# Kernel tuning notes

Hardware: AMD Instinct MI355X
Metric: run time of the kernel (lower is better)

The kernel has to match this reference:

```python
import jax, jax.numpy as jnp
import numpy as np

B, S, D = 4, 16, 512          # batch, seq, attention_dim
V, T = 32000, 18              # vocab_size, tree_depth
INNER = V - 1                 # internal nodes of Huffman tree


def setup_inputs() -> dict:
    key = jax.random.key(0)
    k_att, k_w, k_idx, k_bit = jax.random.split(key, 4)
    att = jax.random.normal(k_att, (B, S, D), dtype=jnp.float32)
    weight = jax.random.normal(k_w, (INNER, D), dtype=jnp.float32) * 0.02
    path_index = jax.random.randint(k_idx, (V * T,), 0, INNER, dtype=jnp.int64)
    # left/right branch bits: sign=+1,bias=0 -> p ; sign=-1,bias=1 -> 1-p
    bits = jax.random.randint(k_bit, (V * T,), 0, 2).astype(jnp.float32)
    path_sign = 1.0 - 2.0 * bits
    path_bias = bits
    return {
        "att": att,
        "weight": weight,
        "path_index": path_index,
        "path_sign": path_sign,
        "path_bias": path_bias,
        "vocab_size": V,
        "tree_depth": T,
    }


def reference(att, weight, path_index, path_sign, path_bias, vocab_size, tree_depth):
    # h: sigmoid of linear projection onto internal-node vectors  [B,S,INNER]
    h = jax.nn.sigmoid(jnp.einsum("bsd,nd->bsn", att, weight))
    # gather per-(token,depth) internal-node probs, flip via sign/bias
    g = jnp.take(h, path_index, axis=-1) * path_sign + path_bias  # [B,S,V*T]
    Hm = g.reshape(att.shape[0], -1, vocab_size, tree_depth)      # [B,S,V,T]
    return jnp.sum(jnp.log(Hm), axis=-1)                          # [B,S,V]
```

## Files before the change

kernel.cpp:

```cpp
#include <hip/hip_runtime.h>
#include <hip/hip_bf16.h>

#define BS    64
#define DDIM  512
#define NV    32000
#define TD    18
#define INNER 31999
#define NPAD  32000

typedef __attribute__((ext_vector_type(8))) short short8;
typedef __attribute__((ext_vector_type(4))) float floatx4;

__device__ __forceinline__ float bf16_to_f32(unsigned short u) {
    union { unsigned int i; float f; } v; v.i = ((unsigned int)u) << 16; return v.f;
}
__device__ __forceinline__ unsigned short f32_to_bf16(float f) {
    union { float f; unsigned int i; } v; v.f = f;
    unsigned int r = v.i + 0x7FFFu + ((v.i >> 16) & 1u);
    return (unsigned short)(r >> 16);
}

__global__ __launch_bounds__(256) void cvt_att(
    const float4* __restrict__ att, ushort4* __restrict__ attb)
{
    int i = blockIdx.x * 256 + threadIdx.x;
    float4 a = att[i];
    ushort4 r;
    r.x = f32_to_bf16(a.x); r.y = f32_to_bf16(a.y);
    r.z = f32_to_bf16(a.z); r.w = f32_to_bf16(a.w);
    attb[i] = r;
}

__global__ __launch_bounds__(512, 4) void gemm_logsig(
    const unsigned short* __restrict__ attb,
    const float* __restrict__ weight,
    unsigned int* __restrict__ pairsT)
{
    __shared__ floatx4 cmb[4][64][4];
    const int tid   = threadIdx.x;
    const int wave  = tid >> 6;
    const int lane  = tid & 63;
    const int ntile = wave & 3;
    const int khalf = wave >> 2;
    const int nb    = blockIdx.x * 64 + ntile * 16;
    const int l15   = lane & 15;
    const int quad  = lane >> 4;

    floatx4 acc[4];
#pragma unroll
    for (int i = 0; i < 4; ++i) acc[i] = (floatx4){0.f, 0.f, 0.f, 0.f};

    int brow = nb + l15;
    if (brow > INNER - 1) brow = INNER - 1;
    const float*          bbase = weight + (size_t)brow * DDIM + khalf * 256 + quad * 8;
    const unsigned short* abase = attb + l15 * DDIM + khalf * 256 + quad * 8;

#pragma unroll 4
    for (int k0 = 0; k0 < 256; k0 += 32) {
        float4 b0 = *(const float4*)(bbase + k0);
        float4 b1 = *(const float4*)(bbase + k0 + 4);
        short8 bfrag;
        bfrag[0] = (short)f32_to_bf16(b0.x); bfrag[1] = (short)f32_to_bf16(b0.y);
        bfrag[2] = (short)f32_to_bf16(b0.z); bfrag[3] = (short)f32_to_bf16(b0.w);
        bfrag[4] = (short)f32_to_bf16(b1.x); bfrag[5] = (short)f32_to_bf16(b1.y);
        bfrag[6] = (short)f32_to_bf16(b1.z); bfrag[7] = (short)f32_to_bf16(b1.w);
#pragma unroll
        for (int mt = 0; mt < 4; ++mt) {
            short8 afrag = *(const short8*)(abase + mt * 16 * DDIM + k0);
            acc[mt] = __builtin_amdgcn_mfma_f32_16x16x32_bf16(afrag, bfrag, acc[mt], 0, 0, 0);
        }
    }

    if (khalf == 1) {
#pragma unroll
        for (int mt = 0; mt < 4; ++mt) cmb[ntile][lane][mt] = acc[mt];
    }
    __syncthreads();
    if (khalf == 0) {
#pragma unroll
        for (int mt = 0; mt < 4; ++mt) acc[mt] += cmb[ntile][lane][mt];

        const int n = nb + l15;
        if (n < INNER) {
            unsigned int* dst = pairsT + (size_t)n * 64 + quad * 4;
#pragma unroll
            for (int mt = 0; mt < 4; ++mt) {
                uint4 pk;
#pragma unroll
                for (int r = 0; r < 4; ++r) {
                    float x = acc[mt][r];
                    float lp = -(fmaxf(-x, 0.f) + __logf(1.f + __expf(-fabsf(x))));
                    float lm = lp - x;
                    ((unsigned int*)&pk)[r] = (unsigned int)f32_to_bf16(lp)
                                            | ((unsigned int)f32_to_bf16(lm) << 16);
                }
                *(uint4*)(dst + mt * 16) = pk;
            }
        }
    }
}

__global__ __launch_bounds__(256) void gather_T(
    const unsigned int* __restrict__ pairsT,
    const int* __restrict__ idx,
    const unsigned int* __restrict__ signbits,
    float* __restrict__ out)
{
    const int lane = threadIdx.x & 63;
    const int wave = threadIdx.x >> 6;

    const unsigned int* w = (const unsigned int*)idx;
    unsigned int orw = 0;
#pragma unroll
    for (int j = 1; j < 16; j += 2) orw |= w[j];
    const bool i64 = (orw == 0u);

#pragma unroll
    for (int g = 0; g < 4; ++g) {
        const int v0 = blockIdx.x * 64 + wave * 16 + g * 4;
        const int i0 = v0 * TD;
        float a0 = 0.f, a1 = 0.f, a2 = 0.f, a3 = 0.f;
#pragma unroll
        for (int t = 0; t < TD; ++t) {
            int j0 = i0 + t, j1 = i0 + TD + t, j2 = i0 + 2 * TD + t, j3 = i0 + 3 * TD + t;
            unsigned int n0 = __builtin_amdgcn_readfirstlane(i64 ? idx[2 * j0] : idx[j0]);
            unsigned int n1 = __builtin_amdgcn_readfirstlane(i64 ? idx[2 * j1] : idx[j1]);
            unsigned int n2 = __builtin_amdgcn_readfirstlane(i64 ? idx[2 * j2] : idx[j2]);
            unsigned int n3 = __builtin_amdgcn_readfirstlane(i64 ? idx[2 * j3] : idx[j3]);
            unsigned int s0 = __builtin_amdgcn_readfirstlane(signbits[j0]) >> 31;
            unsigned int s1 = __builtin_amdgcn_readfirstlane(signbits[j1]) >> 31;
            unsigned int s2 = __builtin_amdgcn_readfirstlane(signbits[j2]) >> 31;
            unsigned int s3 = __builtin_amdgcn_readfirstlane(signbits[j3]) >> 31;
            unsigned int p0 = pairsT[(size_t)n0 * 64 + lane];
            unsigned int p1 = pairsT[(size_t)n1 * 64 + lane];
            unsigned int p2 = pairsT[(size_t)n2 * 64 + lane];
            unsigned int p3 = pairsT[(size_t)n3 * 64 + lane];
            a0 += bf16_to_f32(s0 ? (unsigned short)(p0 >> 16) : (unsigned short)(p0 & 0xFFFFu));
            a1 += bf16_to_f32(s1 ? (unsigned short)(p1 >> 16) : (unsigned short)(p1 & 0xFFFFu));
            a2 += bf16_to_f32(s2 ? (unsigned short)(p2 >> 16) : (unsigned short)(p2 & 0xFFFFu));
            a3 += bf16_to_f32(s3 ? (unsigned short)(p3 >> 16) : (unsigned short)(p3 & 0xFFFFu));
        }
        float4 st = {a0, a1, a2, a3};
        *(float4*)(out + (size_t)lane * NV + v0) = st;
    }
}

extern "C" void kernel_launch(void* const* d_in, const int* in_sizes, int n_in,
                              void* d_out, int out_size, void* d_ws, size_t ws_size,
                              hipStream_t stream)
{
    const float*        att    = (const float*)d_in[0];
    const float*        weight = (const float*)d_in[1];
    const int*          pidx   = (const int*)d_in[2];
    const unsigned int* psign  = (const unsigned int*)d_in[3];
    float* out = (float*)d_out;

    char* ws = (char*)d_ws;
    unsigned int*   pairsT = (unsigned int*)ws;
    unsigned short* attb   = (unsigned short*)(ws + 8192000);

    cvt_att<<<32, 256, 0, stream>>>((const float4*)att, (ushort4*)attb);
    gemm_logsig<<<500, 512, 0, stream>>>(attb, weight, pairsT);
    gather_T<<<500, 256, 0, stream>>>(pairsT, pidx, psign, out);
}
```

Before: 152.7 us.

## Pack path index and sign into 16-bit codes and widen gather batching

A prep kernel, merged with the att-to-bf16 conversion, packs each int64 path index and its sign bit into one 16-bit code. The gather kernel then reads these compact codes instead of separate 8-byte indices and 4-byte sign words. The gather loop is also restructured so each wave issues 16 independent pairsT loads per depth step instead of 4, giving more memory-level parallelism. The cost is an extra pass over the index and sign arrays on every call, plus higher register use in the gather kernel.

```diff
diff --git a/kernel.cpp b/kernel.cpp
--- a/kernel.cpp
+++ b/kernel.cpp
@@ -20,15 +20,31 @@
     return (unsigned short)(r >> 16);
 }
 
-__global__ __launch_bounds__(256) void cvt_att(
-    const float4* __restrict__ att, ushort4* __restrict__ attb)
+#define IDXB 2250
+__global__ __launch_bounds__(256) void prep(
+    const int* __restrict__ idx,
+    const unsigned int* __restrict__ signbits,
+    unsigned short* __restrict__ idx2,
+    const float4* __restrict__ att,
+    ushort4* __restrict__ attb)
 {
-    int i = blockIdx.x * 256 + threadIdx.x;
-    float4 a = att[i];
-    ushort4 r;
-    r.x = f32_to_bf16(a.x); r.y = f32_to_bf16(a.y);
-    r.z = f32_to_bf16(a.z); r.w = f32_to_bf16(a.w);
-    attb[i] = r;
+    const int b = blockIdx.x;
+    if (b < IDXB) {
+        const unsigned int* w = (const unsigned int*)idx;
+        bool i64 = true;
+#pragma unroll
+        for (int j = 1; j < 16; j += 2) i64 &= (w[j] == 0u);
+        int i = b * 256 + threadIdx.x;
+        int val = i64 ? idx[2 * i] : idx[i];
+        idx2[i] = (unsigned short)((val << 1) | (int)(signbits[i] >> 31));
+    } else {
+        int i = (b - IDXB) * 256 + threadIdx.x;
+        float4 a = att[i];
+        ushort4 r;
+        r.x = f32_to_bf16(a.x); r.y = f32_to_bf16(a.y);
+        r.z = f32_to_bf16(a.z); r.w = f32_to_bf16(a.w);
+        attb[i] = r;
+    }
 }
 
 __global__ __launch_bounds__(512, 4) void gemm_logsig(
@@ -102,46 +118,38 @@
 
 __global__ __launch_bounds__(256) void gather_T(
     const unsigned int* __restrict__ pairsT,
-    const int* __restrict__ idx,
-    const unsigned int* __restrict__ signbits,
+    const unsigned short* __restrict__ idx2,
     float* __restrict__ out)
 {
     const int lane = threadIdx.x & 63;
     const int wave = threadIdx.x >> 6;
+    const int v0   = blockIdx.x * 64 + wave * 16;
+    const unsigned short* ip = idx2 + (size_t)v0 * TD;
 
-    const unsigned int* w = (const unsigned int*)idx;
-    unsigned int orw = 0;
+    float acc[16];
 #pragma unroll
-    for (int j = 1; j < 16; j += 2) orw |= w[j];
-    const bool i64 = (orw == 0u);
+    for (int j = 0; j < 16; ++j) acc[j] = 0.f;
+
+#pragma unroll
+    for (int t = 0; t < TD; ++t) {
+        unsigned int e[16];
+        unsigned int p[16];
+#pragma unroll
+        for (int j = 0; j < 16; ++j)
+            e[j] = __builtin_amdgcn_readfirstlane(ip[(size_t)j * TD + t]);
+#pragma unroll
+        for (int j = 0; j < 16; ++j)
+            p[j] = pairsT[(size_t)(e[j] >> 1) * 64 + lane];
+#pragma unroll
+        for (int j = 0; j < 16; ++j)
+            acc[j] += bf16_to_f32((e[j] & 1u) ? (unsigned short)(p[j] >> 16)
+                                              : (unsigned short)(p[j] & 0xFFFFu));
+    }
 
 #pragma unroll
     for (int g = 0; g < 4; ++g) {
-        const int v0 = blockIdx.x * 64 + wave * 16 + g * 4;
-        const int i0 = v0 * TD;
-        float a0 = 0.f, a1 = 0.f, a2 = 0.f, a3 = 0.f;
-#pragma unroll
-        for (int t = 0; t < TD; ++t) {
-            int j0 = i0 + t, j1 = i0 + TD + t, j2 = i0 + 2 * TD + t, j3 = i0 + 3 * TD + t;
-            unsigned int n0 = __builtin_amdgcn_readfirstlane(i64 ? idx[2 * j0] : idx[j0]);
-            unsigned int n1 = __builtin_amdgcn_readfirstlane(i64 ? idx[2 * j1] : idx[j1]);
-            unsigned int n2 = __builtin_amdgcn_readfirstlane(i64 ? idx[2 * j2] : idx[j2]);
-            unsigned int n3 = __builtin_amdgcn_readfirstlane(i64 ? idx[2 * j3] : idx[j3]);
-            unsigned int s0 = __builtin_amdgcn_readfirstlane(signbits[j0]) >> 31;
-            unsigned int s1 = __builtin_amdgcn_readfirstlane(signbits[j1]) >> 31;
-            unsigned int s2 = __builtin_amdgcn_readfirstlane(signbits[j2]) >> 31;
-            unsigned int s3 = __builtin_amdgcn_readfirstlane(signbits[j3]) >> 31;
-            unsigned int p0 = pairsT[(size_t)n0 * 64 + lane];
-            unsigned int p1 = pairsT[(size_t)n1 * 64 + lane];
-            unsigned int p2 = pairsT[(size_t)n2 * 64 + lane];
-            unsigned int p3 = pairsT[(size_t)n3 * 64 + lane];
-            a0 += bf16_to_f32(s0 ? (unsigned short)(p0 >> 16) : (unsigned short)(p0 & 0xFFFFu));
-            a1 += bf16_to_f32(s1 ? (unsigned short)(p1 >> 16) : (unsigned short)(p1 & 0xFFFFu));
-            a2 += bf16_to_f32(s2 ? (unsigned short)(p2 >> 16) : (unsigned short)(p2 & 0xFFFFu));
-            a3 += bf16_to_f32(s3 ? (unsigned short)(p3 >> 16) : (unsigned short)(p3 & 0xFFFFu));
-        }
-        float4 st = {a0, a1, a2, a3};
-        *(float4*)(out + (size_t)lane * NV + v0) = st;
+        float4 st = {acc[g * 4], acc[g * 4 + 1], acc[g * 4 + 2], acc[g * 4 + 3]};
+        *(float4*)(out + (size_t)lane * NV + v0 + g * 4) = st;
     }
 }
 
@@ -157,9 +165,10 @@
 
     char* ws = (char*)d_ws;
     unsigned int*   pairsT = (unsigned int*)ws;
-    unsigned short* attb   = (unsigned short*)(ws + 8192000);
+    unsigned short* idx2   = (unsigned short*)(ws + 8192000);
+    unsigned short* attb   = (unsigned short*)(ws + 9344000);
 
-    cvt_att<<<32, 256, 0, stream>>>((const float4*)att, (ushort4*)attb);
+    prep<<<IDXB + 32, 256, 0, stream>>>(pidx, psign, idx2, (const float4*)att, (ushort4*)attb);
     gemm_logsig<<<500, 512, 0, stream>>>(attb, weight, pairsT);
-    gather_T<<<500, 256, 0, stream>>>(pairsT, pidx, psign, out);
+    gather_T<<<500, 256, 0, stream>>>(pairsT, idx2, out);
 }
```

New measurement: 149.0 us. 1.03x faster.
